# Kernel tuning notes

Hardware: AMD Instinct MI355X
Metric: run time of the kernel (lower is better)

Reference implementation:

```python
import jax, jax.numpy as jnp
import numpy as np

T, H, F, E, K = 4096, 1024, 2048, 8, 2

def setup_inputs() -> dict:
    key = jax.random.key(0)
    k1, k2, k3, k4, k5, k6 = jax.random.split(key, 6)
    scale = 1.0 / np.sqrt(H)
    return {
        "x": jax.random.normal(k1, (T, H), dtype=jnp.float32),
        "expert_ids": jax.random.randint(k2, (T, K), 0, E, dtype=jnp.int32),
        "expert_weights": jax.random.uniform(k3, (T, K), dtype=jnp.float32),
        "gate_weights": jax.random.normal(k4, (E, H, F), dtype=jnp.float32) * scale,
        "up_weights": jax.random.normal(k5, (E, H, F), dtype=jnp.float32) * scale,
        "down_weights": jax.random.normal(k6, (E, F, H), dtype=jnp.float32) * scale,
    }


def reference(x, expert_ids, expert_weights, gate_weights, up_weights, down_weights):
    # Faithful MoE dispatch/combine. The torch module sorts assignments by
    # expert, runs gate/up/down GEMMs per expert on the gathered tokens, and
    # scatter-adds weight * expert_out back per (token, slot) assignment.
    # Equivalent math: for each expert e, each token accumulates
    # (sum of its routing weights for slots routed to e) * FFN_e(x_token).
    num_experts = gate_weights.shape[0]
    out = jnp.zeros_like(x)
    for e in range(num_experts):
        # coeff[t] = sum_k expert_weights[t,k] * (expert_ids[t,k] == e)
        coeff = jnp.sum(jnp.where(expert_ids == e, expert_weights, 0.0), axis=1)  # [T]
        g = x @ gate_weights[e]           # [T, F]
        u = x @ up_weights[e]             # [T, F]
        y = (jax.nn.silu(g) * u) @ down_weights[e]  # [T, H]
        out = out + coeff[:, None] * y
    return out
```

## Files before the change

kernel.cpp:

```cpp
#include <hip/hip_runtime.h>
#include <hip/hip_bf16.h>

#define Td 4096
#define Hd 1024
#define Fd 2048
#define Ed 8

#define BMq 256
#define BNq 128
#define BKq 32

typedef short bf16x8 __attribute__((ext_vector_type(8)));
typedef float f32x4 __attribute__((ext_vector_type(4)));

__device__ __forceinline__ unsigned short f2bf(float f) {
  union { float f; unsigned u; } v; v.f = f;
  unsigned r = v.u + 0x7FFFu + ((v.u >> 16) & 1u);
  return (unsigned short)(r >> 16);
}

__device__ __forceinline__ void gload16(const unsigned short* g, unsigned short* l) {
  __builtin_amdgcn_global_load_lds(
      (const __attribute__((address_space(1))) unsigned int*)g,
      (__attribute__((address_space(3))) unsigned int*)l,
      16, 0, 0);
}

__global__ void xconv_kernel(const float* __restrict__ x, unsigned short* __restrict__ xb) {
  const int i = (blockIdx.x * 256 + threadIdx.x) * 8;
  const float4 v0 = *(const float4*)(x + i);
  const float4 v1 = *(const float4*)(x + i + 4);
  bf16x8 o;
  o[0] = (short)f2bf(v0.x); o[1] = (short)f2bf(v0.y);
  o[2] = (short)f2bf(v0.z); o[3] = (short)f2bf(v0.w);
  o[4] = (short)f2bf(v1.x); o[5] = (short)f2bf(v1.y);
  o[6] = (short)f2bf(v1.z); o[7] = (short)f2bf(v1.w);
  *(bf16x8*)(xb + i) = o;
}

__global__ void prep_transpose_kernel(const float* __restrict__ gw,
                                      const float* __restrict__ uw,
                                      const float* __restrict__ dw,
                                      unsigned short* __restrict__ gu,
                                      unsigned short* __restrict__ dt) {
  const int m = blockIdx.z % 3;
  const int e = blockIdx.z / 3;
  const int R = (m == 2) ? Fd : Hd;
  const int C = (m == 2) ? Hd : Fd;
  const int r0 = blockIdx.y * 64, c0 = blockIdx.x * 64;
  if (r0 >= R || c0 >= C) return;
  const float* src = ((m == 0) ? gw : (m == 1) ? uw : dw) + (size_t)e * Hd * Fd;
  __shared__ unsigned short tile[64][68];
  const int tr = threadIdx.x >> 4;
  const int tc = (threadIdx.x & 15) * 4;
#pragma unroll
  for (int i = 0; i < 4; ++i) {
    const int r = tr + i * 16;
    const float4 v = *(const float4*)(src + (size_t)(r0 + r) * C + c0 + tc);
    tile[r][tc + 0] = f2bf(v.x);
    tile[r][tc + 1] = f2bf(v.y);
    tile[r][tc + 2] = f2bf(v.z);
    tile[r][tc + 3] = f2bf(v.w);
  }
  __syncthreads();
#pragma unroll
  for (int i = 0; i < 4; ++i) {
    const int c = tr + i * 16;
    ushort4 o;
    o.x = tile[tc + 0][c];
    o.y = tile[tc + 1][c];
    o.z = tile[tc + 2][c];
    o.w = tile[tc + 3][c];
    size_t drow = (m == 2) ? (size_t)(c0 + c) : (size_t)(2 * (c0 + c) + m);
    unsigned short* dst = (m == 2) ? (dt + (size_t)e * Hd * Fd)
                                   : (gu + (size_t)e * 2 * Fd * Hd);
    *(ushort4*)(dst + drow * R + r0 + tc) = o;
  }
}

__global__ void routing_kernel(const int* __restrict__ ids,
                               const float* __restrict__ w,
                               int* __restrict__ cnt, int* __restrict__ base,
                               int* __restrict__ tok, float* __restrict__ cof) {
  __shared__ int lcnt[Ed], lbase[Ed], lpos[Ed];
  const int t = threadIdx.x;
  const int lane = t & 63;
  if (t < Ed) { lcnt[t] = 0; lpos[t] = 0; }
  __syncthreads();
  for (int i = t; i < Td; i += 1024) {
    const int e0 = ids[2 * i], e1 = ids[2 * i + 1];
    const int em = (e1 == e0) ? -1 : e1;
#pragma unroll
    for (int e = 0; e < Ed; ++e) {
      unsigned long long m0 = __ballot(e0 == e);
      unsigned long long m1 = __ballot(em == e);
      int n = __popcll(m0) + __popcll(m1);
      if (lane == 0 && n) atomicAdd(&lcnt[e], n);
    }
  }
  __syncthreads();
  if (t == 0) {
    int s = 0;
    for (int e = 0; e < Ed; ++e) { lbase[e] = s; s += lcnt[e]; }
  }
  __syncthreads();
  const unsigned long long below = (1ull << lane) - 1ull;
  for (int i = t; i < Td; i += 1024) {
    const int e0 = ids[2 * i], e1 = ids[2 * i + 1];
    const float w0 = w[2 * i], w1 = w[2 * i + 1];
    const bool mg = (e1 == e0);
    const int em = mg ? -1 : e1;
#pragma unroll
    for (int e = 0; e < Ed; ++e) {
      unsigned long long m0 = __ballot(e0 == e);
      unsigned long long m1 = __ballot(em == e);
      const int n0 = __popcll(m0);
      const int n = n0 + __popcll(m1);
      int p = 0;
      if (lane == 0 && n) p = atomicAdd(&lpos[e], n);
      p = __shfl(p, 0);
      if (e0 == e) {
        const int r = lbase[e] + p + __popcll(m0 & below);
        tok[r] = i; cof[r] = mg ? (w0 + w1) : w0;
      }
      if (em == e) {
        const int r = lbase[e] + p + n0 + __popcll(m1 & below);
        tok[r] = i; cof[r] = w1;
      }
    }
  }
  __syncthreads();
  if (t < Ed) { cnt[t] = lcnt[t]; base[t] = lbase[t]; }
}


__global__ __launch_bounds__(256, 2)
void gateup_kernel(const unsigned short* __restrict__ xb,
                   const unsigned short* __restrict__ gu_t,
                   const int* __restrict__ cnt, const int* __restrict__ base,
                   const int* __restrict__ tok, const float* __restrict__ cof,
                   unsigned short* __restrict__ act) {
  const int e = blockIdx.z, mt = blockIdx.y, nt = blockIdx.x;
  const int cn = cnt[e];
  if (mt * BMq >= cn) return;
  const int b0 = base[e];

  __shared__ unsigned short A_l[3][BMq * BKq];
  __shared__ unsigned short B_l[3][BNq * BKq];
  __shared__ int tok_l[BMq];
  __shared__ float cof_l[BMq];

  const int tid = threadIdx.x, lane = tid & 63, wave = tid >> 6;
  {
    const int r = mt * BMq + tid;
    tok_l[tid] = (r < cn) ? tok[b0 + r] : tok[b0];
    cof_l[tid] = (r < cn) ? cof[b0 + r] : 0.f;
  }
  __syncthreads();

  const unsigned short* gup = gu_t + (size_t)e * 2 * Fd * Hd + (size_t)(nt * BNq) * Hd;
  const unsigned short* aS[4];
  const unsigned short* bS[2];
#pragma unroll
  for (int j = 0; j < 4; ++j) {
    const int s = tid + j * 256;
    const int row = s >> 2, g = (s & 3) ^ ((row >> 1) & 3);
    aS[j] = xb + (size_t)tok_l[row] * Hd + g * 8;
  }
#pragma unroll
  for (int j = 0; j < 2; ++j) {
    const int s = tid + j * 256;
    const int row = s >> 2, g = (s & 3) ^ ((row >> 1) & 3);
    bS[j] = gup + (size_t)row * Hd + g * 8;
  }
  const int dstA = wave * 512;
  const int dstB = wave * 512;

  const int fr16 = lane & 15, kg = lane >> 4;
  const int wm = wave >> 1, wn = wave & 1;
  int aOff[8], bOff[4];
#pragma unroll
  for (int rf = 0; rf < 8; ++rf) {
    const int r = wm * 128 + rf * 16 + fr16;
    aOff[rf] = r * 32 + ((kg ^ ((r >> 1) & 3)) * 8);
  }
#pragma unroll
  for (int cf = 0; cf < 4; ++cf) {
    const int r = wn * 64 + cf * 16 + fr16;
    bOff[cf] = r * 32 + ((kg ^ ((r >> 1) & 3)) * 8);
  }

  f32x4 acc[8][4];
#pragma unroll
  for (int i = 0; i < 8; ++i)
#pragma unroll
    for (int j = 0; j < 4; ++j) acc[i][j] = (f32x4){0.f, 0.f, 0.f, 0.f};

  const int NT = Hd / BKq;
#pragma unroll
  for (int j = 0; j < 4; ++j) gload16(aS[j] + 0, &A_l[0][j * 2048 + dstA]);
#pragma unroll
  for (int j = 0; j < 2; ++j) gload16(bS[j] + 0, &B_l[0][j * 2048 + dstB]);
#pragma unroll
  for (int j = 0; j < 4; ++j) gload16(aS[j] + BKq, &A_l[1][j * 2048 + dstA]);
#pragma unroll
  for (int j = 0; j < 2; ++j) gload16(bS[j] + BKq, &B_l[1][j * 2048 + dstB]);
  asm volatile("s_waitcnt vmcnt(6)" ::: "memory");
  __builtin_amdgcn_s_barrier();

  for (int t = 0; t < NT; ++t) {
    const int sl = t % 3, sn = (t + 2) % 3;
    const bool st = (t + 2) < NT;
    const int kn = (t + 2) * BKq;
    const unsigned short* Ab = &A_l[sl][0];
    const unsigned short* Bb = &B_l[sl][0];
    bf16x8 av[4], bv[4];
#pragma unroll
    for (int rf = 0; rf < 4; ++rf) av[rf] = *(const bf16x8*)(Ab + aOff[rf]);
#pragma unroll
    for (int cf = 0; cf < 4; ++cf) bv[cf] = *(const bf16x8*)(Bb + bOff[cf]);
    if (st) {
      gload16(aS[0] + kn, &A_l[sn][0 * 2048 + dstA]);
      gload16(aS[1] + kn, &A_l[sn][1 * 2048 + dstA]);
      gload16(bS[0] + kn, &B_l[sn][0 * 2048 + dstB]);
    }
    __builtin_amdgcn_s_barrier();
    asm volatile("s_waitcnt lgkmcnt(0)" ::: "memory");
    __builtin_amdgcn_sched_barrier(0);
    __builtin_amdgcn_s_setprio(1);
#pragma unroll
    for (int rf = 0; rf < 4; ++rf)
#pragma unroll
      for (int cf = 0; cf < 4; ++cf)
        acc[rf][cf] = __builtin_amdgcn_mfma_f32_16x16x32_bf16(av[rf], bv[cf], acc[rf][cf], 0, 0, 0);
    __builtin_amdgcn_s_setprio(0);
    __builtin_amdgcn_s_barrier();
    bf16x8 aw[4];
#pragma unroll
    for (int rf = 0; rf < 4; ++rf) aw[rf] = *(const bf16x8*)(Ab + aOff[4 + rf]);
    if (st) {
      gload16(aS[2] + kn, &A_l[sn][2 * 2048 + dstA]);
      gload16(aS[3] + kn, &A_l[sn][3 * 2048 + dstA]);
      gload16(bS[1] + kn, &B_l[sn][1 * 2048 + dstB]);
    }
    __builtin_amdgcn_s_barrier();
    asm volatile("s_waitcnt lgkmcnt(0)" ::: "memory");
    __builtin_amdgcn_sched_barrier(0);
    __builtin_amdgcn_s_setprio(1);
#pragma unroll
    for (int rf = 0; rf < 4; ++rf)
#pragma unroll
      for (int cf = 0; cf < 4; ++cf)
        acc[4 + rf][cf] = __builtin_amdgcn_mfma_f32_16x16x32_bf16(aw[rf], bv[cf], acc[4 + rf][cf], 0, 0, 0);
    __builtin_amdgcn_s_setprio(0);
    if (t < NT - 2)       asm volatile("s_waitcnt vmcnt(6)" ::: "memory");
    else if (t == NT - 2) asm volatile("s_waitcnt vmcnt(0)" ::: "memory");
    __builtin_amdgcn_s_barrier();
  }

  const int row4 = (lane >> 4) * 4;
  const int colbase = nt * BNq + wn * 64;
#pragma unroll
  for (int rf = 0; rf < 8; ++rf) {
#pragma unroll
    for (int cf = 0; cf < 4; ++cf) {
#pragma unroll
      for (int r = 0; r < 4; ++r) {
        const int rr = wm * 128 + rf * 16 + row4 + r;
        const int grow = mt * BMq + rr;
        const float v = acc[rf][cf][r];
        const float p = __shfl_xor(v, 1);
        const float g = (lane & 1) ? p : v;
        const float u = (lane & 1) ? v : p;
        if (grow < cn && !(lane & 1)) {
          const float a = (g / (1.f + __expf(-g))) * u * cof_l[rr];
          const int col = colbase + cf * 16 + fr16;
          act[(size_t)(b0 + grow) * Fd + (col >> 1)] = f2bf(a);
        }
      }
    }
  }
}

__global__ __launch_bounds__(256, 2)
void down_kernel(const unsigned short* __restrict__ act,
                 const unsigned short* __restrict__ down_t,
                 const int* __restrict__ cnt, const int* __restrict__ base,
                 const int* __restrict__ tok,
                 float* __restrict__ out) {
  const int nt = blockIdx.x & 7, kc = blockIdx.x >> 3;
  const int e = blockIdx.z, mt = blockIdx.y;
  const int cn = cnt[e];
  if (mt * BMq >= cn) return;
  const int b0 = base[e];

  __shared__ unsigned short A_l[3][BMq * BKq];
  __shared__ unsigned short B_l[3][BNq * BKq];
  __shared__ int tok_l[BMq];

  const int tid = threadIdx.x, lane = tid & 63, wave = tid >> 6;
  {
    const int r = mt * BMq + tid;
    tok_l[tid] = (r < cn) ? tok[b0 + r] : tok[b0];
  }
  __syncthreads();

  const int kbase = kc * (Fd / 2);
  const unsigned short* dwp = down_t + (size_t)e * Hd * Fd + (size_t)(nt * BNq) * Fd + kbase;
  const unsigned short* aS[4];
  const unsigned short* bS[2];
#pragma unroll
  for (int j = 0; j < 4; ++j) {
    const int s = tid + j * 256;
    const int row = s >> 2, g = (s & 3) ^ ((row >> 1) & 3);
    int ar = b0 + mt * BMq + row;
    if (ar > 8191) ar = 8191;
    aS[j] = act + (size_t)ar * Fd + kbase + g * 8;
  }
#pragma unroll
  for (int j = 0; j < 2; ++j) {
    const int s = tid + j * 256;
    const int row = s >> 2, g = (s & 3) ^ ((row >> 1) & 3);
    bS[j] = dwp + (size_t)row * Fd + g * 8;
  }
  const int dstA = wave * 512, dstB = wave * 512;

  const int fr16 = lane & 15, kg = lane >> 4;
  const int wm = wave >> 1, wn = wave & 1;
  int aOff[8], bOff[4];
#pragma unroll
  for (int rf = 0; rf < 8; ++rf) {
    const int r = wm * 128 + rf * 16 + fr16;
    aOff[rf] = r * 32 + ((kg ^ ((r >> 1) & 3)) * 8);
  }
#pragma unroll
  for (int cf = 0; cf < 4; ++cf) {
    const int r = wn * 64 + cf * 16 + fr16;
    bOff[cf] = r * 32 + ((kg ^ ((r >> 1) & 3)) * 8);
  }

  f32x4 acc[8][4];
#pragma unroll
  for (int i = 0; i < 8; ++i)
#pragma unroll
    for (int j = 0; j < 4; ++j) acc[i][j] = (f32x4){0.f, 0.f, 0.f, 0.f};

  const int NT = (Fd / 2) / BKq;
#pragma unroll
  for (int j = 0; j < 4; ++j) gload16(aS[j] + 0, &A_l[0][j * 2048 + dstA]);
#pragma unroll
  for (int j = 0; j < 2; ++j) gload16(bS[j] + 0, &B_l[0][j * 2048 + dstB]);
#pragma unroll
  for (int j = 0; j < 4; ++j) gload16(aS[j] + BKq, &A_l[1][j * 2048 + dstA]);
#pragma unroll
  for (int j = 0; j < 2; ++j) gload16(bS[j] + BKq, &B_l[1][j * 2048 + dstB]);
  asm volatile("s_waitcnt vmcnt(6)" ::: "memory");
  __builtin_amdgcn_s_barrier();

  for (int t = 0; t < NT; ++t) {
    const int sl = t % 3, sn = (t + 2) % 3;
    const bool st = (t + 2) < NT;
    const int kn = (t + 2) * BKq;
    const unsigned short* Ab = &A_l[sl][0];
    const unsigned short* Bb = &B_l[sl][0];
    bf16x8 av[4], bv[4];
#pragma unroll
    for (int rf = 0; rf < 4; ++rf) av[rf] = *(const bf16x8*)(Ab + aOff[rf]);
#pragma unroll
    for (int cf = 0; cf < 4; ++cf) bv[cf] = *(const bf16x8*)(Bb + bOff[cf]);
    if (st) {
      gload16(aS[0] + kn, &A_l[sn][0 * 2048 + dstA]);
      gload16(aS[1] + kn, &A_l[sn][1 * 2048 + dstA]);
      gload16(bS[0] + kn, &B_l[sn][0 * 2048 + dstB]);
    }
    __builtin_amdgcn_s_barrier();
    asm volatile("s_waitcnt lgkmcnt(0)" ::: "memory");
    __builtin_amdgcn_sched_barrier(0);
    __builtin_amdgcn_s_setprio(1);
#pragma unroll
    for (int rf = 0; rf < 4; ++rf)
#pragma unroll
      for (int cf = 0; cf < 4; ++cf)
        acc[rf][cf] = __builtin_amdgcn_mfma_f32_16x16x32_bf16(av[rf], bv[cf], acc[rf][cf], 0, 0, 0);
    __builtin_amdgcn_s_setprio(0);
    __builtin_amdgcn_s_barrier();
    bf16x8 aw[4];
#pragma unroll
    for (int rf = 0; rf < 4; ++rf) aw[rf] = *(const bf16x8*)(Ab + aOff[4 + rf]);
    if (st) {
      gload16(aS[2] + kn, &A_l[sn][2 * 2048 + dstA]);
      gload16(aS[3] + kn, &A_l[sn][3 * 2048 + dstA]);
      gload16(bS[1] + kn, &B_l[sn][1 * 2048 + dstB]);
    }
    __builtin_amdgcn_s_barrier();
    asm volatile("s_waitcnt lgkmcnt(0)" ::: "memory");
    __builtin_amdgcn_sched_barrier(0);
    __builtin_amdgcn_s_setprio(1);
#pragma unroll
    for (int rf = 0; rf < 4; ++rf)
#pragma unroll
      for (int cf = 0; cf < 4; ++cf)
        acc[4 + rf][cf] = __builtin_amdgcn_mfma_f32_16x16x32_bf16(aw[rf], bv[cf], acc[4 + rf][cf], 0, 0, 0);
    __builtin_amdgcn_s_setprio(0);
    if (t < NT - 2)       asm volatile("s_waitcnt vmcnt(6)" ::: "memory");
    else if (t == NT - 2) asm volatile("s_waitcnt vmcnt(0)" ::: "memory");
    __builtin_amdgcn_s_barrier();
  }

  const int row4 = (lane >> 4) * 4;
  const int colbase = nt * BNq + wn * 64;
#pragma unroll
  for (int rf = 0; rf < 8; ++rf) {
#pragma unroll
    for (int cf = 0; cf < 4; ++cf) {
#pragma unroll
      for (int r = 0; r < 4; ++r) {
        const int rr = wm * 128 + rf * 16 + row4 + r;
        if (mt * BMq + rr < cn) {
          const int col = colbase + cf * 16 + fr16;
          atomicAdd(&out[(size_t)tok_l[rr] * Hd + col], acc[rf][cf][r]);
        }
      }
    }
  }
}

extern "C" void kernel_launch(void* const* d_in, const int* in_sizes, int n_in,
                              void* d_out, int out_size, void* d_ws, size_t ws_size,
                              hipStream_t stream) {
  const float* x  = (const float*)d_in[0];
  const int*   ids = (const int*)d_in[1];
  const float* w  = (const float*)d_in[2];
  const float* gw = (const float*)d_in[3];
  const float* uw = (const float*)d_in[4];
  const float* dw = (const float*)d_in[5];
  float* out = (float*)d_out;

  const size_t SZW = (size_t)Ed * Hd * Fd * 2;
  const size_t ACT = (size_t)8192 * Fd * 2;
  const size_t XB  = (size_t)Td * Hd * 2;
  const size_t NEED = 3 * SZW + ACT + XB + 1 * 1024 * 1024;
  if (ws_size < NEED) return;

  char* ws = (char*)d_ws;
  unsigned short* gu   = (unsigned short*)(ws);
  unsigned short* dt   = (unsigned short*)(ws + 2 * SZW);
  unsigned short* act  = (unsigned short*)(ws + 3 * SZW);
  unsigned short* xbuf = (unsigned short*)(ws + 3 * SZW + ACT);
  char* meta = ws + 3 * SZW + ACT + XB;
  int*   cnt  = (int*)meta;
  int*   base = (int*)(meta + 32);
  int*   tok  = (int*)(meta + 64);
  float* cof  = (float*)(meta + 64 + 8192 * 4);

  hipMemsetAsync(d_out, 0, (size_t)Td * Hd * 4, stream);
  xconv_kernel<<<Td * Hd / 8 / 256, 256, 0, stream>>>(x, xbuf);
  routing_kernel<<<1, 1024, 0, stream>>>(ids, w, cnt, base, tok, cof);
  prep_transpose_kernel<<<dim3(32, 32, 24), 256, 0, stream>>>(gw, uw, dw, gu, dt);
  gateup_kernel<<<dim3(2 * Fd / BNq, Td * 2 / BMq, Ed), 256, 0, stream>>>(xbuf, gu, cnt, base, tok, cof, act);
  down_kernel<<<dim3((Hd / BNq) * 2, Td * 2 / BMq, Ed), 256, 0, stream>>>(act, dt, cnt, base, tok, out);
}
```

Before: 428.6 us.

## Use 256x256 tiles, 512-thread blocks, 4-stage pipeline and compact tile list

The gate/up and down GEMMs now use 256x256 output tiles with 8 waves per block and a 4-deep LDS pipeline instead of 256x128 tiles, 4 waves and a 3-deep pipeline. The routing kernel also builds a compact list of (expert, row-block) tiles, so the grid launches only MAXT row tiles rather than a per-expert grid in which most blocks exit early. The larger tiles raise arithmetic intensity and cut redundant reloads of the gathered A rows. In exchange each block uses much more LDS (about 128KB), which may limit blocks per CU, and the grid has fewer blocks.

```diff
diff --git a/kernel.cpp b/kernel.cpp
--- a/kernel.cpp
+++ b/kernel.cpp
@@ -7,8 +7,9 @@
 #define Ed 8
 
 #define BMq 256
-#define BNq 128
+#define BNq 256
 #define BKq 32
+#define MAXT 40
 
 typedef short bf16x8 __attribute__((ext_vector_type(8)));
 typedef float f32x4 __attribute__((ext_vector_type(4)));
@@ -81,7 +82,9 @@
 __global__ void routing_kernel(const int* __restrict__ ids,
                                const float* __restrict__ w,
                                int* __restrict__ cnt, int* __restrict__ base,
-                               int* __restrict__ tok, float* __restrict__ cof) {
+                               int* __restrict__ tok, float* __restrict__ cof,
+                               int* __restrict__ tle, int* __restrict__ tlrb,
+                               int* __restrict__ ntile) {
   __shared__ int lcnt[Ed], lbase[Ed], lpos[Ed];
   const int t = threadIdx.x;
   const int lane = t & 63;
@@ -100,8 +103,12 @@
   }
   __syncthreads();
   if (t == 0) {
-    int s = 0;
-    for (int e = 0; e < Ed; ++e) { lbase[e] = s; s += lcnt[e]; }
+    int s = 0, nt = 0;
+    for (int e = 0; e < Ed; ++e) {
+      lbase[e] = s; s += lcnt[e];
+      for (int rb = 0; rb < lcnt[e]; rb += BMq) { tle[nt] = e; tlrb[nt] = rb; ++nt; }
+    }
+    *ntile = nt;
   }
   __syncthreads();
   const unsigned long long below = (1ull << lane) - 1ull;
@@ -134,50 +141,46 @@
 }
 
 
-__global__ __launch_bounds__(256, 2)
+__global__ __launch_bounds__(512, 2)
 void gateup_kernel(const unsigned short* __restrict__ xb,
                    const unsigned short* __restrict__ gu_t,
                    const int* __restrict__ cnt, const int* __restrict__ base,
                    const int* __restrict__ tok, const float* __restrict__ cof,
+                   const int* __restrict__ tle, const int* __restrict__ tlrb,
+                   const int* __restrict__ ntile,
                    unsigned short* __restrict__ act) {
-  const int e = blockIdx.z, mt = blockIdx.y, nt = blockIdx.x;
-  const int cn = cnt[e];
-  if (mt * BMq >= cn) return;
-  const int b0 = base[e];
-
-  __shared__ unsigned short A_l[3][BMq * BKq];
-  __shared__ unsigned short B_l[3][BNq * BKq];
+  const int mt = blockIdx.y;
+  if (mt >= *ntile) return;
+  const int e = tle[mt], rb = tlrb[mt], nt = blockIdx.x;
+  const int cn = cnt[e], b0 = base[e];
+
+  __shared__ unsigned short A_l[4][BMq * BKq];
+  __shared__ unsigned short B_l[4][BNq * BKq];
   __shared__ int tok_l[BMq];
   __shared__ float cof_l[BMq];
 
   const int tid = threadIdx.x, lane = tid & 63, wave = tid >> 6;
-  {
-    const int r = mt * BMq + tid;
+  if (tid < BMq) {
+    const int r = rb + tid;
     tok_l[tid] = (r < cn) ? tok[b0 + r] : tok[b0];
     cof_l[tid] = (r < cn) ? cof[b0 + r] : 0.f;
   }
   __syncthreads();
 
   const unsigned short* gup = gu_t + (size_t)e * 2 * Fd * Hd + (size_t)(nt * BNq) * Hd;
-  const unsigned short* aS[4];
+  const unsigned short* aS[2];
   const unsigned short* bS[2];
 #pragma unroll
-  for (int j = 0; j < 4; ++j) {
-    const int s = tid + j * 256;
+  for (int j = 0; j < 2; ++j) {
+    const int s = tid + j * 512;
     const int row = s >> 2, g = (s & 3) ^ ((row >> 1) & 3);
     aS[j] = xb + (size_t)tok_l[row] * Hd + g * 8;
-  }
-#pragma unroll
-  for (int j = 0; j < 2; ++j) {
-    const int s = tid + j * 256;
-    const int row = s >> 2, g = (s & 3) ^ ((row >> 1) & 3);
     bS[j] = gup + (size_t)row * Hd + g * 8;
   }
-  const int dstA = wave * 512;
-  const int dstB = wave * 512;
+  const int dst0 = wave * 512;
 
   const int fr16 = lane & 15, kg = lane >> 4;
-  const int wm = wave >> 1, wn = wave & 1;
+  const int wm = wave >> 2, wn = wave & 3;
   int aOff[8], bOff[4];
 #pragma unroll
   for (int rf = 0; rf < 8; ++rf) {
@@ -198,20 +201,19 @@
 
   const int NT = Hd / BKq;
 #pragma unroll
-  for (int j = 0; j < 4; ++j) gload16(aS[j] + 0, &A_l[0][j * 2048 + dstA]);
-#pragma unroll
-  for (int j = 0; j < 2; ++j) gload16(bS[j] + 0, &B_l[0][j * 2048 + dstB]);
-#pragma unroll
-  for (int j = 0; j < 4; ++j) gload16(aS[j] + BKq, &A_l[1][j * 2048 + dstA]);
-#pragma unroll
-  for (int j = 0; j < 2; ++j) gload16(bS[j] + BKq, &B_l[1][j * 2048 + dstB]);
-  asm volatile("s_waitcnt vmcnt(6)" ::: "memory");
+  for (int p = 0; p < 3; ++p) {
+#pragma unroll
+    for (int j = 0; j < 2; ++j) gload16(aS[j] + p * BKq, &A_l[p][dst0 + j * 4096]);
+#pragma unroll
+    for (int j = 0; j < 2; ++j) gload16(bS[j] + p * BKq, &B_l[p][dst0 + j * 4096]);
+  }
+  asm volatile("s_waitcnt vmcnt(8)" ::: "memory");
   __builtin_amdgcn_s_barrier();
 
   for (int t = 0; t < NT; ++t) {
-    const int sl = t % 3, sn = (t + 2) % 3;
-    const bool st = (t + 2) < NT;
-    const int kn = (t + 2) * BKq;
+    const int sl = t & 3, sn = (t + 3) & 3;
+    const bool st = (t + 3) < NT;
+    const int kn = (t + 3) * BKq;
     const unsigned short* Ab = &A_l[sl][0];
     const unsigned short* Bb = &B_l[sl][0];
     bf16x8 av[4], bv[4];
@@ -220,9 +222,8 @@
 #pragma unroll
     for (int cf = 0; cf < 4; ++cf) bv[cf] = *(const bf16x8*)(Bb + bOff[cf]);
     if (st) {
-      gload16(aS[0] + kn, &A_l[sn][0 * 2048 + dstA]);
-      gload16(aS[1] + kn, &A_l[sn][1 * 2048 + dstA]);
-      gload16(bS[0] + kn, &B_l[sn][0 * 2048 + dstB]);
+      gload16(aS[0] + kn, &A_l[sn][dst0]);
+      gload16(aS[1] + kn, &A_l[sn][dst0 + 4096]);
     }
     __builtin_amdgcn_s_barrier();
     asm volatile("s_waitcnt lgkmcnt(0)" ::: "memory");
@@ -239,9 +240,8 @@
 #pragma unroll
     for (int rf = 0; rf < 4; ++rf) aw[rf] = *(const bf16x8*)(Ab + aOff[4 + rf]);
     if (st) {
-      gload16(aS[2] + kn, &A_l[sn][2 * 2048 + dstA]);
-      gload16(aS[3] + kn, &A_l[sn][3 * 2048 + dstA]);
-      gload16(bS[1] + kn, &B_l[sn][1 * 2048 + dstB]);
+      gload16(bS[0] + kn, &B_l[sn][dst0]);
+      gload16(bS[1] + kn, &B_l[sn][dst0 + 4096]);
     }
     __builtin_amdgcn_s_barrier();
     asm volatile("s_waitcnt lgkmcnt(0)" ::: "memory");
@@ -253,8 +253,9 @@
       for (int cf = 0; cf < 4; ++cf)
         acc[4 + rf][cf] = __builtin_amdgcn_mfma_f32_16x16x32_bf16(aw[rf], bv[cf], acc[4 + rf][cf], 0, 0, 0);
     __builtin_amdgcn_s_setprio(0);
-    if (t < NT - 2)       asm volatile("s_waitcnt vmcnt(6)" ::: "memory");
-    else if (t == NT - 2) asm volatile("s_waitcnt vmcnt(0)" ::: "memory");
+    if (st)                   asm volatile("s_waitcnt vmcnt(8)" ::: "memory");
+    else if ((t + 2) < NT)    asm volatile("s_waitcnt vmcnt(4)" ::: "memory");
+    else if ((t + 1) < NT)    asm volatile("s_waitcnt vmcnt(0)" ::: "memory");
     __builtin_amdgcn_s_barrier();
   }
 
@@ -267,7 +268,7 @@
 #pragma unroll
       for (int r = 0; r < 4; ++r) {
         const int rr = wm * 128 + rf * 16 + row4 + r;
-        const int grow = mt * BMq + rr;
+        const int grow = rb + rr;
         const float v = acc[rf][cf][r];
         const float p = __shfl_xor(v, 1);
         const float g = (lane & 1) ? p : v;
@@ -282,51 +283,48 @@
   }
 }
 
-__global__ __launch_bounds__(256, 2)
+__global__ __launch_bounds__(512, 2)
 void down_kernel(const unsigned short* __restrict__ act,
                  const unsigned short* __restrict__ down_t,
                  const int* __restrict__ cnt, const int* __restrict__ base,
                  const int* __restrict__ tok,
+                 const int* __restrict__ tle, const int* __restrict__ tlrb,
+                 const int* __restrict__ ntile,
                  float* __restrict__ out) {
-  const int nt = blockIdx.x & 7, kc = blockIdx.x >> 3;
-  const int e = blockIdx.z, mt = blockIdx.y;
-  const int cn = cnt[e];
-  if (mt * BMq >= cn) return;
-  const int b0 = base[e];
-
-  __shared__ unsigned short A_l[3][BMq * BKq];
-  __shared__ unsigned short B_l[3][BNq * BKq];
+  const int mt = blockIdx.y;
+  if (mt >= *ntile) return;
+  const int e = tle[mt], rb = tlrb[mt];
+  const int nt = blockIdx.x & 3, kc = blockIdx.x >> 2;
+  const int cn = cnt[e], b0 = base[e];
+
+  __shared__ unsigned short A_l[4][BMq * BKq];
+  __shared__ unsigned short B_l[4][BNq * BKq];
   __shared__ int tok_l[BMq];
 
   const int tid = threadIdx.x, lane = tid & 63, wave = tid >> 6;
-  {
-    const int r = mt * BMq + tid;
-    tok_l[tid] = (r < cn) ? tok[b0 + r] : tok[b0];
+  if (tid < BMq) {
+    const int r = rb + tid;
+    tok_l[tid] = (r < cn) ? tok[b0 + r] : 0;
   }
   __syncthreads();
 
   const int kbase = kc * (Fd / 2);
   const unsigned short* dwp = down_t + (size_t)e * Hd * Fd + (size_t)(nt * BNq) * Fd + kbase;
-  const unsigned short* aS[4];
+  const unsigned short* aS[2];
   const unsigned short* bS[2];
 #pragma unroll
-  for (int j = 0; j < 4; ++j) {
-    const int s = tid + j * 256;
+  for (int j = 0; j < 2; ++j) {
+    const int s = tid + j * 512;
     const int row = s >> 2, g = (s & 3) ^ ((row >> 1) & 3);
-    int ar = b0 + mt * BMq + row;
+    int ar = b0 + rb + row;
     if (ar > 8191) ar = 8191;
     aS[j] = act + (size_t)ar * Fd + kbase + g * 8;
-  }
-#pragma unroll
-  for (int j = 0; j < 2; ++j) {
-    const int s = tid + j * 256;
-    const int row = s >> 2, g = (s & 3) ^ ((row >> 1) & 3);
     bS[j] = dwp + (size_t)row * Fd + g * 8;
   }
-  const int dstA = wave * 512, dstB = wave * 512;
+  const int dst0 = wave * 512;
 
   const int fr16 = lane & 15, kg = lane >> 4;
-  const int wm = wave >> 1, wn = wave & 1;
+  const int wm = wave >> 2, wn = wave & 3;
   int aOff[8], bOff[4];
 #pragma unroll
   for (int rf = 0; rf < 8; ++rf) {
@@ -347,20 +345,19 @@
 
   const int NT = (Fd / 2) / BKq;
 #pragma unroll
-  for (int j = 0; j < 4; ++j) gload16(aS[j] + 0, &A_l[0][j * 2048 + dstA]);
-#pragma unroll
-  for (int j = 0; j < 2; ++j) gload16(bS[j] + 0, &B_l[0][j * 2048 + dstB]);
-#pragma unroll
-  for (int j = 0; j < 4; ++j) gload16(aS[j] + BKq, &A_l[1][j * 2048 + dstA]);
-#pragma unroll
-  for (int j = 0; j < 2; ++j) gload16(bS[j] + BKq, &B_l[1][j * 2048 + dstB]);
-  asm volatile("s_waitcnt vmcnt(6)" ::: "memory");
+  for (int p = 0; p < 3; ++p) {
+#pragma unroll
+    for (int j = 0; j < 2; ++j) gload16(aS[j] + p * BKq, &A_l[p][dst0 + j * 4096]);
+#pragma unroll
+    for (int j = 0; j < 2; ++j) gload16(bS[j] + p * BKq, &B_l[p][dst0 + j * 4096]);
+  }
+  asm volatile("s_waitcnt vmcnt(8)" ::: "memory");
   __builtin_amdgcn_s_barrier();
 
   for (int t = 0; t < NT; ++t) {
-    const int sl = t % 3, sn = (t + 2) % 3;
-    const bool st = (t + 2) < NT;
-    const int kn = (t + 2) * BKq;
+    const int sl = t & 3, sn = (t + 3) & 3;
+    const bool st = (t + 3) < NT;
+    const int kn = (t + 3) * BKq;
     const unsigned short* Ab = &A_l[sl][0];
     const unsigned short* Bb = &B_l[sl][0];
     bf16x8 av[4], bv[4];
@@ -369,9 +366,8 @@
 #pragma unroll
     for (int cf = 0; cf < 4; ++cf) bv[cf] = *(const bf16x8*)(Bb + bOff[cf]);
     if (st) {
-      gload16(aS[0] + kn, &A_l[sn][0 * 2048 + dstA]);
-      gload16(aS[1] + kn, &A_l[sn][1 * 2048 + dstA]);
-      gload16(bS[0] + kn, &B_l[sn][0 * 2048 + dstB]);
+      gload16(aS[0] + kn, &A_l[sn][dst0]);
+      gload16(aS[1] + kn, &A_l[sn][dst0 + 4096]);
     }
     __builtin_amdgcn_s_barrier();
     asm volatile("s_waitcnt lgkmcnt(0)" ::: "memory");
@@ -388,9 +384,8 @@
 #pragma unroll
     for (int rf = 0; rf < 4; ++rf) aw[rf] = *(const bf16x8*)(Ab + aOff[4 + rf]);
     if (st) {
-      gload16(aS[2] + kn, &A_l[sn][2 * 2048 + dstA]);
-      gload16(aS[3] + kn, &A_l[sn][3 * 2048 + dstA]);
-      gload16(bS[1] + kn, &B_l[sn][1 * 2048 + dstB]);
+      gload16(bS[0] + kn, &B_l[sn][dst0]);
+      gload16(bS[1] + kn, &B_l[sn][dst0 + 4096]);
     }
     __builtin_amdgcn_s_barrier();
     asm volatile("s_waitcnt lgkmcnt(0)" ::: "memory");
@@ -402,8 +397,9 @@
       for (int cf = 0; cf < 4; ++cf)
         acc[4 + rf][cf] = __builtin_amdgcn_mfma_f32_16x16x32_bf16(aw[rf], bv[cf], acc[4 + rf][cf], 0, 0, 0);
     __builtin_amdgcn_s_setprio(0);
-    if (t < NT - 2)       asm volatile("s_waitcnt vmcnt(6)" ::: "memory");
-    else if (t == NT - 2) asm volatile("s_waitcnt vmcnt(0)" ::: "memory");
+    if (st)                   asm volatile("s_waitcnt vmcnt(8)" ::: "memory");
+    else if ((t + 2) < NT)    asm volatile("s_waitcnt vmcnt(4)" ::: "memory");
+    else if ((t + 1) < NT)    asm volatile("s_waitcnt vmcnt(0)" ::: "memory");
     __builtin_amdgcn_s_barrier();
   }
 
@@ -416,7 +412,7 @@
 #pragma unroll
       for (int r = 0; r < 4; ++r) {
         const int rr = wm * 128 + rf * 16 + row4 + r;
-        if (mt * BMq + rr < cn) {
+        if (rb + rr < cn) {
           const int col = colbase + cf * 16 + fr16;
           atomicAdd(&out[(size_t)tok_l[rr] * Hd + col], acc[rf][cf][r]);
         }
@@ -448,15 +444,18 @@
   unsigned short* act  = (unsigned short*)(ws + 3 * SZW);
   unsigned short* xbuf = (unsigned short*)(ws + 3 * SZW + ACT);
   char* meta = ws + 3 * SZW + ACT + XB;
-  int*   cnt  = (int*)meta;
-  int*   base = (int*)(meta + 32);
-  int*   tok  = (int*)(meta + 64);
-  float* cof  = (float*)(meta + 64 + 8192 * 4);
+  int*   cnt   = (int*)meta;
+  int*   base  = (int*)(meta + 32);
+  int*   tok   = (int*)(meta + 64);
+  float* cof   = (float*)(meta + 64 + 8192 * 4);
+  int*   tle   = (int*)(meta + 64 + 8192 * 8);
+  int*   tlrb  = (int*)(meta + 64 + 8192 * 8 + MAXT * 4);
+  int*   ntile = (int*)(meta + 64 + 8192 * 8 + 2 * MAXT * 4);
 
   hipMemsetAsync(d_out, 0, (size_t)Td * Hd * 4, stream);
   xconv_kernel<<<Td * Hd / 8 / 256, 256, 0, stream>>>(x, xbuf);
-  routing_kernel<<<1, 1024, 0, stream>>>(ids, w, cnt, base, tok, cof);
+  routing_kernel<<<1, 1024, 0, stream>>>(ids, w, cnt, base, tok, cof, tle, tlrb, ntile);
   prep_transpose_kernel<<<dim3(32, 32, 24), 256, 0, stream>>>(gw, uw, dw, gu, dt);
-  gateup_kernel<<<dim3(2 * Fd / BNq, Td * 2 / BMq, Ed), 256, 0, stream>>>(xbuf, gu, cnt, base, tok, cof, act);
-  down_kernel<<<dim3((Hd / BNq) * 2, Td * 2 / BMq, Ed), 256, 0, stream>>>(act, dt, cnt, base, tok, out);
-}
+  gateup_kernel<<<dim3(2 * Fd / BNq, MAXT), 512, 0, stream>>>(xbuf, gu, cnt, base, tok, cof, tle, tlrb, ntile, act);
+  down_kernel<<<dim3((Hd / BNq) * 2, MAXT), 512, 0, stream>>>(act, dt, cnt, base, tok, tle, tlrb, ntile, out);
+}
```

Measured after the change: 424.9 us. About the same (-0.9%).
